# Kernel optimization log

Measured on AMD Instinct MI355X. Metric: run time of the kernel, lower is better.

The kernel has to match this reference:

```python
import jax, jax.numpy as jnp
import numpy as np

N_SEL = 8192      # total nodes across selected subgraphs
SUB_SZ = 32       # nodes per subgraph
N_SUB = 256       # number of subgraphs (N_SEL / SUB_SZ)
N_GRAPH = 64      # source graphs (4 subgraphs each)
N_FULL = 12288    # nodes in the full graph
E_RAW = 262144    # raw edges
N_PERS = 4        # weighted-cosine perspectives
D = 128           # feature dim
EPSILON = 0.1
LAMB1 = 0.5


def setup_inputs() -> dict:
    key = jax.random.key(0)
    k1, k2, k3, k4, k5 = jax.random.split(key, 5)
    x = jax.random.normal(k1, (N_SEL, D), dtype=jnp.float32)
    Wc = jax.random.normal(k2, (N_PERS, D), dtype=jnp.float32)
    selected_score = jax.random.uniform(k3, (N_SUB,), dtype=jnp.float32) + 0.1
    selected_batch = jnp.asarray(np.arange(N_SEL) // SUB_SZ, dtype=jnp.int32)
    selected_belong = jnp.asarray(np.arange(N_SUB) // (N_SUB // N_GRAPH), dtype=jnp.int32)
    # injective mapping from selected nodes -> full-graph node ids
    selected_mapping = jax.random.permutation(k4, N_FULL)[:N_SEL].astype(jnp.int32)
    # block-diagonal complete edge set within each subgraph (torch.meshgrid in prepare_parsed_data)
    base = (np.arange(N_SUB) * SUB_SZ)[:, None, None]
    r = np.broadcast_to(np.arange(SUB_SZ)[None, :, None], (N_SUB, SUB_SZ, SUB_SZ)) + base
    c = np.broadcast_to(np.arange(SUB_SZ)[None, None, :], (N_SUB, SUB_SZ, SUB_SZ)) + base
    full_edge_index = jnp.asarray(np.stack([r.ravel(), c.ravel()]), dtype=jnp.int32)
    raw_edge_index = jax.random.randint(k5, (2, E_RAW), 0, N_FULL, dtype=jnp.int32)
    return {"x": x, "Wc": Wc, "selected_score": selected_score,
            "selected_batch": selected_batch, "selected_mapping": selected_mapping,
            "selected_belong": selected_belong, "full_edge_index": full_edge_index,
            "raw_edge_index": raw_edge_index}


def reference(x, Wc, selected_score, selected_batch, selected_mapping,
              selected_belong, full_edge_index, raw_edge_index):
    # ---- per-graph scatter-normalization of subgraph scores ----
    score_sum = jax.ops.segment_sum(selected_score, selected_belong, num_segments=N_GRAPH)
    score = selected_score / score_sum[selected_belong]          # [N_SUB]

    # ---- WeightedCosine metric: dense pairwise adjacency over all selected nodes ----
    h = x[None, :, :] * Wc[:, None, :]                            # [P, N_sel, D]
    hn = h / jnp.clip(jnp.linalg.norm(h, axis=-1, keepdims=True), 1e-12)
    adj = jnp.einsum('pid,pjd->ij', hn, hn) / N_PERS              # [N_sel, N_sel]

    # ---- mask to intra-subgraph candidate edges ----
    mask = jnp.zeros((N_SEL, N_SEL), dtype=adj.dtype).at[full_edge_index[0], full_edge_index[1]].set(1.0)
    adj = adj * mask
    # EpsilonNN
    adj = adj * (adj > EPSILON).astype(adj.dtype)
    # RemoveSelfLoop
    adj = adj * (1.0 - jnp.eye(N_SEL, dtype=adj.dtype))
    # dense_to_sparse + weighting: weight each edge by its row-node's subgraph score
    attr = adj * (score[selected_batch] * LAMB1)[:, None]         # [N_sel, N_sel]

    # ---- map to full-graph ids and coalesce (duplicate-sum) into dense adjacency ----
    out = jnp.zeros((N_FULL, N_FULL), dtype=x.dtype)
    out = out.at[selected_mapping[:, None], selected_mapping[None, :]].add(attr)
    out = out.at[raw_edge_index[0], raw_edge_index[1]].add(1.0 - LAMB1)
    return out
```

## Files before the change

### kernel.cpp

```cpp
#include <hip/hip_runtime.h>

#define N_SEL 8192
#define SUB_SZ 32
#define N_SUB 256
#define N_GRAPH 64
#define N_FULL 12288
#define E_RAW 262144
#define N_PERS 4
#define D 128
#define EPSILON 0.1f
#define LAMB1 0.5f

__global__ __launch_bounds__(256) void subgraph_kernel(
        const float* __restrict__ x,
        const float* __restrict__ Wc,
        const float* __restrict__ sscore,
        const int*   __restrict__ smap,
        float* __restrict__ out)
{
    const int s    = blockIdx.x;
    const int base = s * SUB_SZ;
    const int tid  = threadIdx.x;

    __shared__ float xs[SUB_SZ][D + 1];
    __shared__ float w2[N_PERS][D];
    __shared__ float rnorm[N_PERS][SUB_SZ];
    __shared__ int   map_s[SUB_SZ];
    __shared__ float rowscore;

    for (int k = tid; k < SUB_SZ * D; k += 256) {
        int i = k >> 7;
        int d = k & (D - 1);
        xs[i][d] = x[(base + i) * D + d];
    }
    for (int k = tid; k < N_PERS * D; k += 256) {
        float w = Wc[k];
        ((float*)w2)[k] = w * w;
    }
    if (tid < SUB_SZ) map_s[tid] = smap[base + tid];
    if (tid == 0) {
        int g4 = (s >> 2) << 2;
        float sum = sscore[g4] + sscore[g4 + 1] + sscore[g4 + 2] + sscore[g4 + 3];
        rowscore = (sscore[s] / sum) * LAMB1;
    }
    __syncthreads();

    if (tid < N_PERS * SUB_SZ) {
        int p = tid >> 5;
        int i = tid & 31;
        float acc = 0.f;
        #pragma unroll 8
        for (int d = 0; d < D; ++d) {
            float v = xs[i][d];
            acc = fmaf(v * v, w2[p][d], acc);
        }
        float n = fmaxf(sqrtf(acc), 1e-12f);
        rnorm[p][i] = 1.0f / n;
    }
    __syncthreads();

    for (int e = tid; e < SUB_SZ * SUB_SZ; e += 256) {
        int i = e >> 5;
        int j = e & 31;
        if (i == j) continue;
        float a0 = 0.f, a1 = 0.f, a2 = 0.f, a3 = 0.f;
        #pragma unroll 8
        for (int d = 0; d < D; ++d) {
            float prod = xs[i][d] * xs[j][d];
            a0 = fmaf(prod, w2[0][d], a0);
            a1 = fmaf(prod, w2[1][d], a1);
            a2 = fmaf(prod, w2[2][d], a2);
            a3 = fmaf(prod, w2[3][d], a3);
        }
        float adj = 0.25f * (a0 * rnorm[0][i] * rnorm[0][j] +
                             a1 * rnorm[1][i] * rnorm[1][j] +
                             a2 * rnorm[2][i] * rnorm[2][j] +
                             a3 * rnorm[3][i] * rnorm[3][j]);
        if (adj > EPSILON) {
            long long row = map_s[i];
            long long col = map_s[j];
            out[row * (long long)N_FULL + col] = adj * rowscore;
        }
    }
}

__global__ __launch_bounds__(256) void raw_edge_kernel(
        const int* __restrict__ ei, float* __restrict__ out)
{
    int e = blockIdx.x * blockDim.x + threadIdx.x;
    if (e < E_RAW) {
        long long r = ei[e];
        long long c = ei[E_RAW + e];
        atomicAdd(&out[r * (long long)N_FULL + c], 1.0f - LAMB1);
    }
}

extern "C" void kernel_launch(void* const* d_in, const int* in_sizes, int n_in,
                              void* d_out, int out_size, void* d_ws, size_t ws_size,
                              hipStream_t stream) {
    const float* x      = (const float*)d_in[0];
    const float* Wc     = (const float*)d_in[1];
    const float* sscore = (const float*)d_in[2];
    const int* smap = (const int*)d_in[4];
    const int* rei  = (const int*)d_in[7];
    float* out = (float*)d_out;

    hipMemsetAsync(out, 0, (size_t)out_size * sizeof(float), stream);

    subgraph_kernel<<<N_SUB, 256, 0, stream>>>(x, Wc, sscore, smap, out);

    raw_edge_kernel<<<E_RAW / 256, 256, 0, stream>>>(rei, out);
}
```

Baseline: 168.8 us.

## Replace memset with nontemporal vector zero kernel and fuse scatter kernels

Replaces hipMemsetAsync with a custom kernel that zeroes the output using float4 nontemporal stores, each block filling a fixed contiguous chunk. The subgraph and raw-edge scatter kernels are merged into one launch. Because the two scatters can now run concurrently on the same addresses, the subgraph writes switch from plain stores to atomicAdd. This removes one launch and the gap between kernels, at the cost of extra atomic traffic on the subgraph writes.

```diff
diff --git a/kernel.cpp b/kernel.cpp
--- a/kernel.cpp
+++ b/kernel.cpp
@@ -11,16 +11,42 @@
 #define EPSILON 0.1f
 #define LAMB1 0.5f
 
-__global__ __launch_bounds__(256) void subgraph_kernel(
+#define N4_TOTAL 37748736
+#define FILL_BLOCKS 4096
+#define PER_BLOCK (N4_TOTAL / FILL_BLOCKS)
+#define FILL_ITERS (PER_BLOCK / 256)
+
+typedef float f4_t __attribute__((ext_vector_type(4)));
+
+__global__ __launch_bounds__(256) void zero_kernel(f4_t* __restrict__ out)
+{
+    size_t base = (size_t)blockIdx.x * PER_BLOCK + threadIdx.x;
+    const f4_t z = (f4_t){0.f, 0.f, 0.f, 0.f};
+    #pragma unroll
+    for (int k = 0; k < FILL_ITERS; ++k)
+        __builtin_nontemporal_store(z, &out[base + (size_t)k * 256]);
+}
+
+__global__ __launch_bounds__(256) void scatter_kernel(
         const float* __restrict__ x,
         const float* __restrict__ Wc,
         const float* __restrict__ sscore,
         const int*   __restrict__ smap,
+        const int*   __restrict__ rei,
         float* __restrict__ out)
 {
+    const int tid = threadIdx.x;
+
+    if (blockIdx.x >= N_SUB) {
+        int e = (blockIdx.x - N_SUB) * 256 + tid;
+        long long r = rei[e];
+        long long c = rei[E_RAW + e];
+        atomicAdd(&out[r * (long long)N_FULL + c], 1.0f - LAMB1);
+        return;
+    }
+
     const int s    = blockIdx.x;
     const int base = s * SUB_SZ;
-    const int tid  = threadIdx.x;
 
     __shared__ float xs[SUB_SZ][D + 1];
     __shared__ float w2[N_PERS][D];
@@ -54,8 +80,7 @@
             float v = xs[i][d];
             acc = fmaf(v * v, w2[p][d], acc);
         }
-        float n = fmaxf(sqrtf(acc), 1e-12f);
-        rnorm[p][i] = 1.0f / n;
+        rnorm[p][i] = 1.0f / fmaxf(sqrtf(acc), 1e-12f);
     }
     __syncthreads();
 
@@ -79,19 +104,8 @@
         if (adj > EPSILON) {
             long long row = map_s[i];
             long long col = map_s[j];
-            out[row * (long long)N_FULL + col] = adj * rowscore;
+            atomicAdd(&out[row * (long long)N_FULL + col], adj * rowscore);
         }
-    }
-}
-
-__global__ __launch_bounds__(256) void raw_edge_kernel(
-        const int* __restrict__ ei, float* __restrict__ out)
-{
-    int e = blockIdx.x * blockDim.x + threadIdx.x;
-    if (e < E_RAW) {
-        long long r = ei[e];
-        long long c = ei[E_RAW + e];
-        atomicAdd(&out[r * (long long)N_FULL + c], 1.0f - LAMB1);
     }
 }
 
@@ -105,9 +119,7 @@
     const int* rei  = (const int*)d_in[7];
     float* out = (float*)d_out;
 
-    hipMemsetAsync(out, 0, (size_t)out_size * sizeof(float), stream);
+    zero_kernel<<<FILL_BLOCKS, 256, 0, stream>>>((f4_t*)out);
 
-    subgraph_kernel<<<N_SUB, 256, 0, stream>>>(x, Wc, sscore, smap, out);
-
-    raw_edge_kernel<<<E_RAW / 256, 256, 0, stream>>>(rei, out);
+    scatter_kernel<<<N_SUB + E_RAW / 256, 256, 0, stream>>>(x, Wc, sscore, smap, rei, out);
 }
```

Result: faster. 160.3 us (-5.1%).
